# Performance work log

Measured on AMD Instinct MI355X. Metric: run time of the kernel, lower is better.

## Reference

```python
import jax, jax.numpy as jnp
import numpy as np

B, L, D = 128, 196, 512
T = 20
V, E, H, A = 10000, 256, 512, 512


def setup_inputs() -> dict:
    key = jax.random.key(0)
    ks = jax.random.split(key, 20)
    s = lambda *sh: 0.02
    inp = {
        "a": jax.random.normal(ks[0], (B, L, D), jnp.float32),
        "captions": jax.random.randint(ks[1], (B, T), 0, V),
        "lengths": jnp.full((B,), T, dtype=jnp.int64),
        "embed_W": jax.random.normal(ks[2], (V, E), jnp.float32) * 0.02,
        "Wa": jax.random.normal(ks[3], (D, A), jnp.float32) * 0.02,
        "Wh": jax.random.normal(ks[4], (H, A), jnp.float32) * 0.02,
        "Wc": jax.random.normal(ks[5], (H, A), jnp.float32) * 0.02,
        "v": jax.random.normal(ks[6], (A,), jnp.float32) * 0.02,
        "beta_W": jax.random.normal(ks[7], (H, 1), jnp.float32) * 0.02,
        "beta_b": jnp.zeros((1,), jnp.float32),
        "W_ih": jax.random.normal(ks[8], (E + D, 4 * H), jnp.float32) * 0.02,
        "W_hh": jax.random.normal(ks[9], (H, 4 * H), jnp.float32) * 0.02,
        "b_ih": jnp.zeros((4 * H,), jnp.float32),
        "b_hh": jnp.zeros((4 * H,), jnp.float32),
        "fc_W": jax.random.normal(ks[10], (H, V), jnp.float32) * 0.02,
        "fc_b": jnp.zeros((V,), jnp.float32),
        "initW_h": jax.random.normal(ks[11], (D, H), jnp.float32) * 0.02,
        "initb_h": jnp.zeros((H,), jnp.float32),
        "initW_c": jax.random.normal(ks[12], (D, H), jnp.float32) * 0.02,
        "initb_c": jnp.zeros((H,), jnp.float32),
    }
    return inp


def _decode(a, captions, embed_W, Wa, Wh, Wc, v, beta_W, beta_b,
            W_ih, W_hh, b_ih, b_hh, fc_W, fc_b,
            initW_h, initb_h, initW_c, initb_c):
    # dropout layers are treated as identity (eval mode) for a deterministic reference
    emb = embed_W[captions]                       # (B, T, E)
    mean_ctx = a.mean(axis=1)                     # (B, D)
    h0 = jnp.tanh(mean_ctx @ initW_h + initb_h)   # (B, H)
    c0 = jnp.tanh(mean_ctx @ initW_c + initb_c)
    wa = a @ Wa                                   # (B, L, A), hoisted (invariant over t)
    Hd = h0.shape[-1]

    def step(carry, x_t):
        h, c, prev_h = carry
        # dual additive attention: scores from annotations + h + prev_h (context_input)
        score = jnp.tanh(wa + (h @ Wh)[:, None, :] + (prev_h @ Wc)[:, None, :])  # (B,L,A)
        e = score @ v                                                            # (B,L)
        alpha = jax.nn.softmax(e, axis=1)
        beta = jax.nn.sigmoid(h @ beta_W + beta_b)                               # (B,1)
        ctx = beta * jnp.einsum('bl,bld->bd', alpha, a)                          # (B,D)
        # LSTMCell
        x = jnp.concatenate([x_t, ctx], axis=1)                                  # (B,E+D)
        gates = x @ W_ih + b_ih + h @ W_hh + b_hh                                # (B,4H)
        i, f, g, o = jnp.split(gates, 4, axis=1)
        c_new = jax.nn.sigmoid(f) * c + jax.nn.sigmoid(i) * jnp.tanh(g)
        h_new = jax.nn.sigmoid(o) * jnp.tanh(c_new)
        logits_t = h_new @ fc_W + fc_b                                           # (B,V)
        return (h_new, c_new, h_new), (logits_t, alpha)

    xs = jnp.swapaxes(emb[:, :T - 1, :], 0, 1)    # (T-1, B, E) time-major
    _, (logits_t, alphas_t) = jax.lax.scan(step, (h0, c0, h0), xs)
    # all lengths == T: pack_padded_sequence(batch_first=True).data is time-major flatten
    packed_logits = logits_t.reshape((T - 1) * a.shape[0], -1)                   # ((T-1)*B, V)
    alphas = jnp.swapaxes(alphas_t, 0, 1)                                        # (B, T-1, L)
    return packed_logits, alphas


def reference(a, captions, lengths, embed_W, Wa, Wh, Wc, v, beta_W, beta_b,
              W_ih, W_hh, b_ih, b_hh, fc_W, fc_b,
              initW_h, initb_h, initW_c, initb_c):
    return _decode(a, captions, embed_W, Wa, Wh, Wc, v, beta_W, beta_b,
                   W_ih, W_hh, b_ih, b_hh, fc_W, fc_b,
                   initW_h, initb_h, initW_c, initb_c)
```

## Files before the change

### kernel.cpp

```cpp
#include <hip/hip_runtime.h>
#include <hip/hip_bf16.h>
#include <math.h>

#define B_ 128
#define L_ 196
#define D_ 512
#define T_ 20
#define V_ 10000
#define E_ 256
#define H_ 512
#define A_ 512
#define TM1 19
#define ROWS (TM1*B_)
#define G4H 2048
#define KCAT 1024
#define LH 98

typedef unsigned short ushort_t;
typedef __attribute__((ext_vector_type(8))) short bf16x8;
typedef __attribute__((ext_vector_type(4))) float f32x4;

__device__ __forceinline__ float fast_tanh(float x){
    float ax = fabsf(x);
    float e = __expf(-2.f*ax);
    float r = __builtin_amdgcn_rcpf(1.f + e);
    return copysignf((1.f - e)*r, x);
}
__device__ __forceinline__ float sigmoidf_(float x){
    return __builtin_amdgcn_rcpf(1.f + __expf(-x));
}
__device__ __forceinline__ ushort_t f2b(float f){
    union{float f; unsigned u;} x; x.f = f;
    unsigned r = x.u + 0x7fffu + ((x.u>>16)&1u);
    return (ushort_t)(r>>16);
}
__device__ __forceinline__ float b2f(ushort_t h){
    union{unsigned u; float f;} x; x.u = ((unsigned)h)<<16;
    return x.f;
}
__device__ __forceinline__ float b2f_lo(unsigned u){ union{unsigned u; float f;} x; x.u = u<<16; return x.f; }
__device__ __forceinline__ float b2f_hi(unsigned u){ union{unsigned u; float f;} x; x.u = u & 0xffff0000u; return x.f; }

#define GL16(gsrc, ldst) __builtin_amdgcn_global_load_lds( \
    (const __attribute__((address_space(1))) unsigned*)(gsrc), \
    (__attribute__((address_space(3))) unsigned*)(ldst), 16, 0, 0)

template<int OUT_BF16, int HAS_BIAS, int NT, int SWZ>
__global__ __launch_bounds__(256)
void gemm_mfma(const ushort_t* __restrict__ A, int lda,
               const ushort_t* __restrict__ BT, int ldb,
               void* __restrict__ Cout, int ldc,
               int N, int K, const float* __restrict__ bias)
{
    __shared__ ushort_t As[2][4096];
    __shared__ ushort_t Bs[2][4096];
    int bm, bn;
    if (SWZ){
        int bid = blockIdx.x;
        int swz = (bid & 7)*190 + (bid >> 3);
        int mt = swz % 19, nt = swz / 19;
        if (nt >= 79) return;
        bm = mt*128; bn = nt*128;
    } else {
        bm = blockIdx.y * 128; bn = blockIdx.x * 128;
    }
    const int tid = threadIdx.x;
    const int lane = tid & 63;
    const int wave = tid >> 6;
    const int wm = (wave >> 1) * 64;
    const int wn = (wave & 1) * 64;
    const int lrow = lane & 15;
    const int lk8  = (lane >> 4) * 8;
    const int srow = tid >> 2;
    const int skq0 = (tid & 3) * 8;
    const int wbase = wave * 512;

    f32x4 acc[4][4];
    #pragma unroll
    for (int i=0;i<4;i++)
        #pragma unroll
        for (int j=0;j<4;j++) acc[i][j] = (f32x4){0.f,0.f,0.f,0.f};

    const ushort_t* Ab = A  + (size_t)(bm+srow)*lda + skq0;
    const ushort_t* Bb = BT + (size_t)(bn+srow)*ldb + skq0;

    GL16(Ab,                    &As[0][wbase]);
    GL16(Ab + (size_t)64*lda,   &As[0][2048 + wbase]);
    GL16(Bb,                    &Bs[0][wbase]);
    GL16(Bb + (size_t)64*ldb,   &Bs[0][2048 + wbase]);

    int buf = 0;
    for (int k0 = 0; k0 < K; k0 += 32) {
        asm volatile("s_waitcnt vmcnt(0)" ::: "memory");
        __syncthreads();
        if (k0 + 32 < K){
            int nb = buf ^ 1;
            GL16(Ab + k0 + 32,                  &As[nb][wbase]);
            GL16(Ab + (size_t)64*lda + k0 + 32, &As[nb][2048 + wbase]);
            GL16(Bb + k0 + 32,                  &Bs[nb][wbase]);
            GL16(Bb + (size_t)64*ldb + k0 + 32, &Bs[nb][2048 + wbase]);
        }
        bf16x8 af[4], bfr[4];
        #pragma unroll
        for (int i=0;i<4;i++) af[i]  = *(bf16x8*)&As[buf][(wm + i*16 + lrow)*32 + lk8];
        #pragma unroll
        for (int j=0;j<4;j++) bfr[j] = *(bf16x8*)&Bs[buf][(wn + j*16 + lrow)*32 + lk8];
        #pragma unroll
        for (int i=0;i<4;i++)
            #pragma unroll
            for (int j=0;j<4;j++)
                acc[i][j] = __builtin_amdgcn_mfma_f32_16x16x32_bf16(af[i], bfr[j], acc[i][j], 0, 0, 0);
        buf ^= 1;
    }

    const int rq = (lane >> 4) * 4;
    #pragma unroll
    for (int j=0;j<4;j++){
        int col = bn + wn + j*16 + lrow;
        if (col >= N) continue;
        float bv = HAS_BIAS ? bias[col] : 0.f;
        #pragma unroll
        for (int i=0;i<4;i++){
            #pragma unroll
            for (int q=0;q<4;q++){
                int row = bm + wm + i*16 + rq + q;
                float v = acc[i][j][q] + bv;
                if (OUT_BF16) ((ushort_t*)Cout)[(size_t)row*ldc + col] = f2b(v);
                else if (NT)  __builtin_nontemporal_store(v, &((float*)Cout)[(size_t)row*ldc + col]);
                else          ((float*)Cout)[(size_t)row*ldc + col] = v;
            }
        }
    }
}

__global__ __launch_bounds__(256) void gemm64t2(const float* __restrict__ A, int lda,
                       const float* __restrict__ B0, const float* __restrict__ B1, int ldb,
                       float* __restrict__ C0, float* __restrict__ C1, int ldc,
                       const float* __restrict__ bias0, const float* __restrict__ bias1)
{
    const float* Bm  = blockIdx.z ? B1 : B0;
    float* C         = blockIdx.z ? C1 : C0;
    const float* bias= blockIdx.z ? bias1 : bias0;
    __shared__ float As[16][65];
    __shared__ float Bs[16][65];
    int bm = blockIdx.y*64, bn = blockIdx.x*64;
    int tid = threadIdx.x;
    int tx = tid & 15, ty = tid >> 4;
    float acc[4][4] = {};
    for (int k0 = 0; k0 < D_; k0 += 16) {
        {
            int r  = tid >> 2;
            int kq = (tid & 3) * 4;
            float4 va = *(const float4*)(A + (size_t)(bm+r)*lda + k0 + kq);
            As[kq+0][r]=va.x; As[kq+1][r]=va.y; As[kq+2][r]=va.z; As[kq+3][r]=va.w;
        }
        {
            int kk = tid >> 4;
            int nq = (tid & 15) * 4;
            float4 vb = *(const float4*)(Bm + (size_t)(k0+kk)*ldb + bn + nq);
            Bs[kk][nq+0]=vb.x; Bs[kk][nq+1]=vb.y; Bs[kk][nq+2]=vb.z; Bs[kk][nq+3]=vb.w;
        }
        __syncthreads();
        #pragma unroll
        for (int k = 0; k < 16; ++k) {
            float a0[4], b0[4];
            #pragma unroll
            for (int i=0;i<4;i++) a0[i] = As[k][ty*4+i];
            #pragma unroll
            for (int j=0;j<4;j++) b0[j] = Bs[k][tx*4+j];
            #pragma unroll
            for (int i=0;i<4;i++)
                #pragma unroll
                for (int j=0;j<4;j++)
                    acc[i][j] = fmaf(a0[i], b0[j], acc[i][j]);
        }
        __syncthreads();
    }
    #pragma unroll
    for (int i=0;i<4;i++){
        int row = bm + ty*4 + i;
        #pragma unroll
        for (int j=0;j<4;j++){
            int col = bn + tx*4 + j;
            C[(size_t)row*ldc + col] = fast_tanh(acc[i][j] + bias[col]);
        }
    }
}

struct TJob { const float* src; const float* src2; ushort_t* dst;
              int lds, Ksz, Nsz, koff, ldk, nx, nblk; };
struct TJobs { TJob j[6]; };

__global__ __launch_bounds__(256) void combo_trans_k(TJobs J){
    __shared__ float t[32][33];
    int bid = blockIdx.x;
    int ji = 0;
    while (bid >= J.j[ji].nblk){ bid -= J.j[ji].nblk; ji++; }
    const TJob jb = J.j[ji];
    int n0 = (bid % jb.nx)*32, k0 = (bid / jb.nx)*32;
    int tx = threadIdx.x & 31, ty = threadIdx.x >> 5;
    #pragma unroll
    for (int kk = ty; kk < 32; kk += 8){
        int k = k0 + kk, n = n0 + tx;
        float v = 0.f;
        if (k < jb.Ksz && n < jb.Nsz){
            v = jb.src[(size_t)k*jb.lds + n];
            if (jb.src2) v += jb.src2[(size_t)k*jb.lds + n];
        }
        t[kk][tx] = v;
    }
    __syncthreads();
    #pragma unroll
    for (int nn = ty; nn < 32; nn += 8){
        int n = n0 + nn, k = k0 + tx;
        if (k < jb.Ksz) jb.dst[(size_t)n*jb.ldk + jb.koff + k] = f2b(t[tx][nn]);
    }
}

__global__ __launch_bounds__(256) void mean_cvt_k(const float* __restrict__ a, ushort_t* __restrict__ a_b,
                                                  float* __restrict__ mc,
                                                  const float* __restrict__ b_ih, const float* __restrict__ b_hh,
                                                  float* __restrict__ bias4h, unsigned* __restrict__ ebar){
    if (blockIdx.x == 64){
        for (int k = threadIdx.x; k < G4H; k += 256) bias4h[k] = b_ih[k] + b_hh[k];
        if (threadIdx.x < B_) ebar[threadIdx.x] = 0u;
        return;
    }
    int idx = blockIdx.x*256 + threadIdx.x;
    int b = idx >> 7, dq = (idx & 127) * 4;
    const float* p = a + (size_t)b*L_*D_ + dq;
    ushort_t* q = a_b + (size_t)b*L_*D_ + dq;
    float4 s = make_float4(0.f,0.f,0.f,0.f);
    for (int l=0;l<L_;l++){
        float4 v = *(const float4*)(p + (size_t)l*D_);
        s.x += v.x; s.y += v.y; s.z += v.z; s.w += v.w;
        ushort_t r[4] = {f2b(v.x),f2b(v.y),f2b(v.z),f2b(v.w)};
        *(uint2*)(q + (size_t)l*D_) = *(uint2*)r;
    }
    const float inv = 1.f/(float)L_;
    float4 o = make_float4(s.x*inv, s.y*inv, s.z*inv, s.w*inv);
    *(float4*)(mc + (size_t)b*D_ + dq) = o;
}

__global__ __launch_bounds__(256) void gather_emb(const int* __restrict__ captions, const float* __restrict__ embW,
                           ushort_t* __restrict__ xemb){
    int i = blockIdx.x*4 + (threadIdx.x >> 6);
    int lane = threadIdx.x & 63;
    int t = i / B_, b = i - t*B_;
    int cap = captions[b*T_ + t];
    float4 v = ((const float4*)(embW + (size_t)cap*E_))[lane];
    ushort_t r[4] = {f2b(v.x),f2b(v.y),f2b(v.z),f2b(v.w)};
    *(uint2*)(xemb + (size_t)i*E_ + lane*4) = *(uint2*)r;
}

__global__ __launch_bounds__(512) void hw0cvt_k(const float* __restrict__ h0f,
                        const ushort_t* __restrict__ WhcT,
                        ushort_t* __restrict__ xcat, float* __restrict__ hWp){
    int b = blockIdx.x, tid = threadIdx.x;
    int lane = tid & 63, wave = tid >> 6;
    __shared__ ushort_t hls[512];
    float hv = h0f[b*H_ + tid];
    ushort_t hb = f2b(hv);
    xcat[(size_t)b*KCAT + D_ + tid] = hb;
    hls[tid] = hb;
    hWp[(size_t)(b*2+1)*512 + tid] = 0.f;
    __syncthreads();
    int wn = wave * 64;
    int col16 = lane & 15;
    int khi = (lane >> 4) * 8;
    bool a_on = (col16 == 0);
    f32x4 acc[4];
    #pragma unroll
    for (int f=0;f<4;f++) acc[f] = (f32x4){0.f,0.f,0.f,0.f};
    for (int kk=0; kk<16; kk++){
        bf16x8 af = (bf16x8){0,0,0,0,0,0,0,0};
        if (a_on) af = *(const bf16x8*)&hls[kk*32 + khi];
        #pragma unroll
        for (int f=0;f<4;f++){
            bf16x8 bf = *(const bf16x8*)(WhcT + (size_t)(wn + f*16 + col16)*512 + kk*32 + khi);
            acc[f] = __builtin_amdgcn_mfma_f32_16x16x32_bf16(af, bf, acc[f], 0, 0, 0);
        }
    }
    if (lane < 16){
        #pragma unroll
        for (int f=0;f<4;f++) hWp[(size_t)(b*2+0)*512 + wn + f*16 + lane] = acc[f][0];
    }
}

__global__ __launch_bounds__(512) void mega2_k(const ushort_t* __restrict__ wa,
                        const ushort_t* __restrict__ a_b,
                        const float* __restrict__ v,
                        const float* __restrict__ beta_W, const float* __restrict__ beta_b,
                        const ushort_t* __restrict__ WhcT,
                        const float* __restrict__ gp, const float* __restrict__ embWih,
                        float* __restrict__ cbuf, float* __restrict__ hWp,
                        ushort_t* __restrict__ xcat, ushort_t* __restrict__ Hall,
                        float* __restrict__ alphas_out, float* __restrict__ ebuf,
                        unsigned* __restrict__ ebar, int t)
{
    const int b = blockIdx.x, half = blockIdx.y;
    const int tid = threadIdx.x;
    const int lane = tid & 63, wave = tid >> 6;
    __shared__ ushort_t hls[256];
    __shared__ float red[512];
    __shared__ float al_s[224];
    __shared__ float part[2][256];

    if (t > 0){
        if (tid < 256){
            const int j = half*256 + tid;
            const float* eb = embWih + ((size_t)((t-1)*B_ + b))*G4H;
            float gi = eb[j], gf = eb[H_+j], gg = eb[2*H_+j], go = eb[3*H_+j];
            #pragma unroll
            for (int ks=0; ks<8; ks++){
                const float* g = gp + ((size_t)(ks*B_ + b))*G4H;
                gi += g[j]; gf += g[H_+j]; gg += g[2*H_+j]; go += g[3*H_+j];
            }
            float ig = sigmoidf_(gi), fg = sigmoidf_(gf);
            float g2 = fast_tanh(gg), og = sigmoidf_(go);
            float c = fg*cbuf[b*H_+j] + ig*g2;
            float h = og*fast_tanh(c);
            cbuf[b*H_+j] = c;
            ushort_t hb = f2b(h);
            xcat[(size_t)b*KCAT + D_ + j] = hb;
            Hall[((size_t)(t-1)*B_ + b)*H_ + j] = hb;
            hls[tid] = hb;
        }
        __syncthreads();
        int wn = wave * 64;
        int col16 = lane & 15;
        int khi = (lane >> 4) * 8;
        bool a_on = (col16 == 0);
        f32x4 acc[4];
        #pragma unroll
        for (int f=0;f<4;f++) acc[f] = (f32x4){0.f,0.f,0.f,0.f};
        #pragma unroll
        for (int kk=0; kk<8; kk++){
            bf16x8 af = (bf16x8){0,0,0,0,0,0,0,0};
            if (a_on) af = *(const bf16x8*)&hls[kk*32 + khi];
            #pragma unroll
            for (int f=0;f<4;f++){
                bf16x8 bf = *(const bf16x8*)(WhcT + (size_t)(wn + f*16 + col16)*512 + half*256 + kk*32 + khi);
                acc[f] = __builtin_amdgcn_mfma_f32_16x16x32_bf16(af, bf, acc[f], 0, 0, 0);
            }
        }
        if (lane < 16){
            #pragma unroll
            for (int f=0;f<4;f++) hWp[(size_t)(b*2+half)*512 + wn + f*16 + lane] = acc[f][0];
        }
    }
    __syncthreads();
    if (tid == 0){
        __threadfence();
        atomicAdd(&ebar[b], 1u);
        const unsigned tgt = 2u*(unsigned)(2*t+1);
        while (__hip_atomic_load(&ebar[b], __ATOMIC_ACQUIRE, __HIP_MEMORY_SCOPE_AGENT) < tgt)
            __builtin_amdgcn_s_sleep(1);
    }
    __syncthreads();
    {
        const float* hp0 = hWp + (size_t)(b*2+0)*512 + lane*8;
        const float* hp1 = hWp + (size_t)(b*2+1)*512 + lane*8;
        float4 p00 = *(const float4*)hp0, p01 = *(const float4*)(hp0+4);
        float4 p10 = *(const float4*)hp1, p11 = *(const float4*)(hp1+4);
        float4 hw0 = make_float4(p00.x+p10.x, p00.y+p10.y, p00.z+p10.z, p00.w+p10.w);
        float4 hw1 = make_float4(p01.x+p11.x, p01.y+p11.y, p01.z+p11.z, p01.w+p11.w);
        const float* vp = v + lane*8;
        float4 v0 = *(const float4*)vp, v1 = *(const float4*)(vp+4);
        const int l0 = half*LH;
        for (int r = wave; r < LH; r += 8){
            int4 raw = *(const int4*)(wa + (((size_t)(b*L_ + l0 + r))<<9) + lane*8);
            const unsigned* u = (const unsigned*)&raw;
            float s;
            s  = fast_tanh(b2f_lo(u[0]) + hw0.x)*v0.x;
            s += fast_tanh(b2f_hi(u[0]) + hw0.y)*v0.y;
            s += fast_tanh(b2f_lo(u[1]) + hw0.z)*v0.z;
            s += fast_tanh(b2f_hi(u[1]) + hw0.w)*v0.w;
            s += fast_tanh(b2f_lo(u[2]) + hw1.x)*v1.x;
            s += fast_tanh(b2f_hi(u[2]) + hw1.y)*v1.y;
            s += fast_tanh(b2f_lo(u[3]) + hw1.z)*v1.z;
            s += fast_tanh(b2f_hi(u[3]) + hw1.w)*v1.w;
            #pragma unroll
            for (int off=32; off; off>>=1) s += __shfl_down(s, off);
            if (lane==0) ebuf[b*L_ + l0 + r] = s;
        }
    }
    __syncthreads();
    if (tid == 0){
        __threadfence();
        atomicAdd(&ebar[b], 1u);
        const unsigned tgt = 2u*(unsigned)(2*t+2);
        while (__hip_atomic_load(&ebar[b], __ATOMIC_ACQUIRE, __HIP_MEMORY_SCOPE_AGENT) < tgt)
            __builtin_amdgcn_s_sleep(1);
    }
    __syncthreads();
    float ev = (tid < L_) ? ebuf[b*L_ + tid] : -3.0e38f;
    red[tid] = ev; __syncthreads();
    #pragma unroll
    for (int s=256; s; s>>=1){ if (tid<s) red[tid] = fmaxf(red[tid], red[tid+s]); __syncthreads(); }
    float m = red[0]; __syncthreads();
    float pr = (tid < L_) ? __expf(ev - m) : 0.f;
    red[tid] = pr; __syncthreads();
    #pragma unroll
    for (int s=256; s; s>>=1){ if (tid<s) red[tid] += red[tid+s]; __syncthreads(); }
    float inv = 1.f / red[0];
    __syncthreads();
    if (tid < L_) al_s[tid] = pr*inv;
    const int l0 = half*LH;
    if (tid >= l0 && tid < l0 + LH)
        __builtin_nontemporal_store(pr*inv, alphas_out + (size_t)b*TM1*L_ + (size_t)t*L_ + tid);
    float dv = b2f(xcat[(size_t)b*KCAT + D_ + tid]) * beta_W[tid];
    red[tid] = dv; __syncthreads();
    #pragma unroll
    for (int s=256; s; s>>=1){ if (tid<s) red[tid] += red[tid+s]; __syncthreads(); }
    float beta = sigmoidf_(red[0] + beta_b[0]);
    __syncthreads();
    const int d  = half*256 + (tid & 255);
    const int lr = tid >> 8;
    const ushort_t* pa = a_b + (((size_t)(b*L_ + lr*LH))<<9) + d;
    float s0 = 0.f;
    #pragma unroll 7
    for (int i=0; i<LH; ++i) s0 = fmaf(al_s[lr*LH + i], b2f(pa[(size_t)i*512]), s0);
    part[lr][tid & 255] = s0;
    __syncthreads();
    if (tid < 256)
        xcat[(size_t)b*KCAT + half*256 + tid] = f2b(beta*(part[0][tid] + part[1][tid]));
}

__global__ __launch_bounds__(256) void gates_k(const ushort_t* __restrict__ xcat,
                        const ushort_t* __restrict__ WcatT, float* __restrict__ gp){
    __shared__ ushort_t As[128*32];
    __shared__ ushort_t Bs[64*32];
    const int bn = blockIdx.x*64;
    const int ks = blockIdx.y;
    const int tid = threadIdx.x;
    const int lane = tid & 63, wave = tid >> 6;
    const int wm = wave*32;
    const int lrow = lane & 15;
    const int lk8 = (lane >> 4) * 8;
    f32x4 acc[2][4];
    #pragma unroll
    for (int i=0;i<2;i++)
        #pragma unroll
        for (int j=0;j<4;j++) acc[i][j] = (f32x4){0.f,0.f,0.f,0.f};

    for (int kk = 0; kk < 4; ++kk){
        int k0 = ks*128 + kk*32;
        int c0 = 2*tid;
        int r0 = c0 >> 2,  kq0 = (c0 & 3)*8;
        int r1 = (c0+1) >> 2, kq1 = ((c0+1) & 3)*8;
        int4 a0 = *(const int4*)(xcat + (size_t)r0*KCAT + k0 + kq0);
        int4 a1 = *(const int4*)(xcat + (size_t)r1*KCAT + k0 + kq1);
        int rb = tid >> 2, kqb = (tid & 3)*8;
        int4 b0 = *(const int4*)(WcatT + (size_t)(bn+rb)*KCAT + k0 + kqb);
        __syncthreads();
        *(int4*)&As[r0*32 + kq0] = a0;
        *(int4*)&As[r1*32 + kq1] = a1;
        *(int4*)&Bs[rb*32 + kqb] = b0;
        __syncthreads();
        bf16x8 af[2], bfr[4];
        #pragma unroll
        for (int i=0;i<2;i++) af[i] = *(bf16x8*)&As[(wm + i*16 + lrow)*32 + lk8];
        #pragma unroll
        for (int j=0;j<4;j++) bfr[j] = *(bf16x8*)&Bs[(j*16 + lrow)*32 + lk8];
        #pragma unroll
        for (int i=0;i<2;i++)
            #pragma unroll
            for (int j=0;j<4;j++)
                acc[i][j] = __builtin_amdgcn_mfma_f32_16x16x32_bf16(af[i], bfr[j], acc[i][j], 0, 0, 0);
    }
    const int rq = (lane >> 4) * 4;
    #pragma unroll
    for (int i=0;i<2;i++){
        #pragma unroll
        for (int j=0;j<4;j++){
            int gcol = bn + j*16 + lrow;
            #pragma unroll
            for (int q=0;q<4;q++){
                int grow = wm + i*16 + rq + q;
                gp[((size_t)(ks*B_ + grow))*G4H + gcol] = acc[i][j][q];
            }
        }
    }
}

__global__ __launch_bounds__(512) void lstmfin_k(const float* __restrict__ gp, const float* __restrict__ embWih,
                       const float* __restrict__ cbuf, ushort_t* __restrict__ Hall){
    int b = blockIdx.x, j = threadIdx.x;
    const float* eb = embWih + ((size_t)(18*B_ + b))*G4H;
    float gi = eb[j], gf = eb[H_+j], gg = eb[2*H_+j], go = eb[3*H_+j];
    #pragma unroll
    for (int ks=0; ks<8; ks++){
        const float* g = gp + ((size_t)(ks*B_ + b))*G4H;
        gi += g[j]; gf += g[H_+j]; gg += g[2*H_+j]; go += g[3*H_+j];
    }
    float ig = sigmoidf_(gi), fg = sigmoidf_(gf);
    float g2 = fast_tanh(gg), og = sigmoidf_(go);
    float c = fg*cbuf[b*H_+j] + ig*g2;
    float h = og*fast_tanh(c);
    Hall[((size_t)18*B_ + b)*H_ + j] = f2b(h);
}

extern "C" void kernel_launch(void* const* d_in, const int* in_sizes, int n_in,
                              void* d_out, int out_size, void* d_ws, size_t ws_size,
                              hipStream_t stream) {
    const float* a      = (const float*)d_in[0];
    const int*   caps   = (const int*)  d_in[1];
    const float* embW   = (const float*)d_in[3];
    const float* Wa     = (const float*)d_in[4];
    const float* Wh     = (const float*)d_in[5];
    const float* Wc     = (const float*)d_in[6];
    const float* v      = (const float*)d_in[7];
    const float* beta_W = (const float*)d_in[8];
    const float* beta_b = (const float*)d_in[9];
    const float* W_ih   = (const float*)d_in[10];
    const float* W_hh   = (const float*)d_in[11];
    const float* b_ih   = (const float*)d_in[12];
    const float* b_hh   = (const float*)d_in[13];
    const float* fc_W   = (const float*)d_in[14];
    const float* fc_b   = (const float*)d_in[15];
    const float* iWh    = (const float*)d_in[16];
    const float* ibh    = (const float*)d_in[17];
    const float* iWc    = (const float*)d_in[18];
    const float* ibc    = (const float*)d_in[19];

    float* out    = (float*)d_out;
    float* alphas = out + (size_t)ROWS*V_;

    char* ob = (char*)d_out;
    ushort_t* wa_b   = (ushort_t*)(ob);
    ushort_t* a_b    = (ushort_t*)(ob + 25690112);
    float*    embWih = (float*)   (ob + 51380224);

    char* wb = (char*)d_ws;
    float* mean_ctx = (float*)(wb);
    float* cbuf     = (float*)(wb + 262144);
    float* h0f      = (float*)(wb + 524288);
    float* hWp      = (float*)(wb + 786432);
    float* ebuf     = (float*)(wb + 1310720);
    float* bias4h   = (float*)(wb + 1413120);
    unsigned* ebar  = (unsigned*)(wb + 1421312);
    float* gp       = (float*)(wb + 1422336);
    ushort_t* xcat_b = (ushort_t*)(wb + 9810944);
    ushort_t* xemb_b = (ushort_t*)(wb + 10073088);
    ushort_t* Hall   = (ushort_t*)(wb + 11318272);
    ushort_t* WaT    = (ushort_t*)(wb + 13808640);
    ushort_t* WhcT   = (ushort_t*)(wb + 14332928);
    ushort_t* WihT   = (ushort_t*)(wb + 14857216);
    ushort_t* WcatT  = (ushort_t*)(wb + 15905792);
    ushort_t* fcWT   = (ushort_t*)(wb + 20100096);

    TJobs J;
    J.j[0] = { Wa,   nullptr, WaT,  512, 512, 512,  0,   512,  16, 256 };
    J.j[1] = { Wh,   Wc,      WhcT, 512, 512, 512,  0,   512,  16, 256 };
    J.j[2] = { W_ih, nullptr, WihT, G4H, 256, G4H,  0,   256,  64, 512 };
    J.j[3] = { W_ih + (size_t)E_*G4H, nullptr, WcatT, G4H, 512, G4H, 0,   KCAT, 64, 1024 };
    J.j[4] = { W_hh, nullptr, WcatT, G4H, 512, G4H,  512, KCAT, 64, 1024 };
    J.j[5] = { fc_W, nullptr, fcWT, V_,  512, V_,   0,   512,  316, 5056 };
    combo_trans_k<<<8128, 256, 0, stream>>>(J);
    mean_cvt_k<<<65, 256, 0, stream>>>(a, a_b, mean_ctx, b_ih, b_hh, bias4h, ebar);
    gather_emb<<<ROWS/4, 256, 0, stream>>>(caps, embW, xemb_b);
    gemm64t2<<<dim3(8,2,2), 256, 0, stream>>>(mean_ctx, D_, iWh, iWc, H_, h0f, cbuf, H_, ibh, ibc);
    hw0cvt_k<<<B_, 512, 0, stream>>>(h0f, WhcT, xcat_b, hWp);
    gemm_mfma<1,0,0,0><<<dim3(4,196), 256, 0, stream>>>(a_b, D_, WaT, D_, wa_b, A_, A_, D_, nullptr);
    gemm_mfma<0,1,0,0><<<dim3(16,19), 256, 0, stream>>>(xemb_b, E_, WihT, E_, embWih, G4H, G4H, E_, bias4h);

    for (int t = 0; t < TM1; ++t){
        mega2_k<<<dim3(B_,2), 512, 0, stream>>>(wa_b, a_b, v, beta_W, beta_b, WhcT,
                                                gp, embWih, cbuf, hWp, xcat_b, Hall,
                                                alphas, ebuf, ebar, t);
        gates_k<<<dim3(32,8), 256, 0, stream>>>(xcat_b, WcatT, gp);
    }
    lstmfin_k<<<B_, 512, 0, stream>>>(gp, embWih, cbuf, Hall);

    gemm_mfma<0,1,1,1><<<dim3(1520), 256, 0, stream>>>(Hall, H_, fcWT, H_, out, V_, V_, H_, fc_b);
}
```

Before: 1.063 ms.

## Fuse prep kernels and dual GEMMs; replace tree reductions with shuffles in attention step

Merges the transpose, mean/convert and embedding-gather kernels into one launch, and runs the Wa and embedding-input GEMMs as one dual-job launch, to cut launch overhead and fill the GPU better. Inside the recurrent step kernel, the beta gate dot product now comes from per-half partials computed while h is produced, and the max/sum softmax reductions use wave shuffles instead of 512-wide shared-memory trees. The context weighted sum reads four values per vectorized load with eight row groups. This adds cross-block dependency handling for the beta partials and more complex indexing.

```diff
diff --git a/kernel.cpp b/kernel.cpp
--- a/kernel.cpp
+++ b/kernel.cpp
@@ -128,6 +128,84 @@
                 if (OUT_BF16) ((ushort_t*)Cout)[(size_t)row*ldc + col] = f2b(v);
                 else if (NT)  __builtin_nontemporal_store(v, &((float*)Cout)[(size_t)row*ldc + col]);
                 else          ((float*)Cout)[(size_t)row*ldc + col] = v;
+            }
+        }
+    }
+}
+
+struct GJob { const ushort_t* A; int lda; const ushort_t* BT; int ldb;
+              void* C; int ldc; int N, K; const float* bias; int out_bf16; int nx; int nblk; };
+
+__global__ __launch_bounds__(256) void gemm_dual_k(GJob j0, GJob j1){
+    __shared__ ushort_t As[2][4096];
+    __shared__ ushort_t Bs[2][4096];
+    int bid = blockIdx.x;
+    GJob jb = (bid < j0.nblk) ? j0 : j1;
+    if (bid >= j0.nblk) bid -= j0.nblk;
+    const int bn = (bid % jb.nx)*128, bm = (bid / jb.nx)*128;
+    const int tid = threadIdx.x;
+    const int lane = tid & 63;
+    const int wave = tid >> 6;
+    const int wm = (wave >> 1) * 64;
+    const int wn = (wave & 1) * 64;
+    const int lrow = lane & 15;
+    const int lk8  = (lane >> 4) * 8;
+    const int srow = tid >> 2;
+    const int skq0 = (tid & 3) * 8;
+    const int wbase = wave * 512;
+
+    f32x4 acc[4][4];
+    #pragma unroll
+    for (int i=0;i<4;i++)
+        #pragma unroll
+        for (int j=0;j<4;j++) acc[i][j] = (f32x4){0.f,0.f,0.f,0.f};
+
+    const ushort_t* Ab = jb.A  + (size_t)(bm+srow)*jb.lda + skq0;
+    const ushort_t* Bb = jb.BT + (size_t)(bn+srow)*jb.ldb + skq0;
+
+    GL16(Ab,                        &As[0][wbase]);
+    GL16(Ab + (size_t)64*jb.lda,    &As[0][2048 + wbase]);
+    GL16(Bb,                        &Bs[0][wbase]);
+    GL16(Bb + (size_t)64*jb.ldb,    &Bs[0][2048 + wbase]);
+
+    int buf = 0;
+    for (int k0 = 0; k0 < jb.K; k0 += 32) {
+        asm volatile("s_waitcnt vmcnt(0)" ::: "memory");
+        __syncthreads();
+        if (k0 + 32 < jb.K){
+            int nb = buf ^ 1;
+            GL16(Ab + k0 + 32,                      &As[nb][wbase]);
+            GL16(Ab + (size_t)64*jb.lda + k0 + 32,  &As[nb][2048 + wbase]);
+            GL16(Bb + k0 + 32,                      &Bs[nb][wbase]);
+            GL16(Bb + (size_t)64*jb.ldb + k0 + 32,  &Bs[nb][2048 + wbase]);
+        }
+        bf16x8 af[4], bfr[4];
+        #pragma unroll
+        for (int i=0;i<4;i++) af[i]  = *(bf16x8*)&As[buf][(wm + i*16 + lrow)*32 + lk8];
+        #pragma unroll
+        for (int j=0;j<4;j++) bfr[j] = *(bf16x8*)&Bs[buf][(wn + j*16 + lrow)*32 + lk8];
+        #pragma unroll
+        for (int i=0;i<4;i++)
+            #pragma unroll
+            for (int j=0;j<4;j++)
+                acc[i][j] = __builtin_amdgcn_mfma_f32_16x16x32_bf16(af[i], bfr[j], acc[i][j], 0, 0, 0);
+        buf ^= 1;
+    }
+
+    const int rq = (lane >> 4) * 4;
+    #pragma unroll
+    for (int j=0;j<4;j++){
+        int col = bn + wn + j*16 + lrow;
+        if (col >= jb.N) continue;
+        float bv = jb.bias ? jb.bias[col] : 0.f;
+        #pragma unroll
+        for (int i=0;i<4;i++){
+            #pragma unroll
+            for (int q=0;q<4;q++){
+                int row = bm + wm + i*16 + rq + q;
+                float v = acc[i][j][q] + bv;
+                if (jb.out_bf16) ((ushort_t*)jb.C)[(size_t)row*jb.ldc + col] = f2b(v);
+                else             ((float*)jb.C)[(size_t)row*jb.ldc + col] = v;
             }
         }
     }
@@ -189,82 +267,95 @@
 
 struct TJob { const float* src; const float* src2; ushort_t* dst;
               int lds, Ksz, Nsz, koff, ldk, nx, nblk; };
-struct TJobs { TJob j[6]; };
-
-__global__ __launch_bounds__(256) void combo_trans_k(TJobs J){
+struct PrepArgs {
+    TJob j[6];
+    const float* a; ushort_t* a_b; float* mc;
+    const float* b_ih; const float* b_hh; float* bias4h; unsigned* ebar;
+    const int* caps; const float* embW; ushort_t* xemb;
+};
+
+__global__ __launch_bounds__(256) void prep_all_k(PrepArgs P){
     __shared__ float t[32][33];
     int bid = blockIdx.x;
-    int ji = 0;
-    while (bid >= J.j[ji].nblk){ bid -= J.j[ji].nblk; ji++; }
-    const TJob jb = J.j[ji];
-    int n0 = (bid % jb.nx)*32, k0 = (bid / jb.nx)*32;
-    int tx = threadIdx.x & 31, ty = threadIdx.x >> 5;
-    #pragma unroll
-    for (int kk = ty; kk < 32; kk += 8){
-        int k = k0 + kk, n = n0 + tx;
-        float v = 0.f;
-        if (k < jb.Ksz && n < jb.Nsz){
-            v = jb.src[(size_t)k*jb.lds + n];
-            if (jb.src2) v += jb.src2[(size_t)k*jb.lds + n];
-        }
-        t[kk][tx] = v;
-    }
-    __syncthreads();
-    #pragma unroll
-    for (int nn = ty; nn < 32; nn += 8){
-        int n = n0 + nn, k = k0 + tx;
-        if (k < jb.Ksz) jb.dst[(size_t)n*jb.ldk + jb.koff + k] = f2b(t[tx][nn]);
-    }
-}
-
-__global__ __launch_bounds__(256) void mean_cvt_k(const float* __restrict__ a, ushort_t* __restrict__ a_b,
-                                                  float* __restrict__ mc,
-                                                  const float* __restrict__ b_ih, const float* __restrict__ b_hh,
-                                                  float* __restrict__ bias4h, unsigned* __restrict__ ebar){
-    if (blockIdx.x == 64){
-        for (int k = threadIdx.x; k < G4H; k += 256) bias4h[k] = b_ih[k] + b_hh[k];
-        if (threadIdx.x < B_) ebar[threadIdx.x] = 0u;
+    const int tid = threadIdx.x;
+    if (bid < 8128){
+        int ji = 0;
+        while (bid >= P.j[ji].nblk){ bid -= P.j[ji].nblk; ji++; }
+        const TJob jb = P.j[ji];
+        int n0 = (bid % jb.nx)*32, k0 = (bid / jb.nx)*32;
+        int tx = tid & 31, ty = tid >> 5;
+        #pragma unroll
+        for (int kk = ty; kk < 32; kk += 8){
+            int k = k0 + kk, n = n0 + tx;
+            float v = 0.f;
+            if (k < jb.Ksz && n < jb.Nsz){
+                v = jb.src[(size_t)k*jb.lds + n];
+                if (jb.src2) v += jb.src2[(size_t)k*jb.lds + n];
+            }
+            t[kk][tx] = v;
+        }
+        __syncthreads();
+        #pragma unroll
+        for (int nn = ty; nn < 32; nn += 8){
+            int n = n0 + nn, k = k0 + tx;
+            if (k < jb.Ksz) jb.dst[(size_t)n*jb.ldk + jb.koff + k] = f2b(t[tx][nn]);
+        }
         return;
     }
-    int idx = blockIdx.x*256 + threadIdx.x;
-    int b = idx >> 7, dq = (idx & 127) * 4;
-    const float* p = a + (size_t)b*L_*D_ + dq;
-    ushort_t* q = a_b + (size_t)b*L_*D_ + dq;
-    float4 s = make_float4(0.f,0.f,0.f,0.f);
-    for (int l=0;l<L_;l++){
-        float4 v = *(const float4*)(p + (size_t)l*D_);
-        s.x += v.x; s.y += v.y; s.z += v.z; s.w += v.w;
-        ushort_t r[4] = {f2b(v.x),f2b(v.y),f2b(v.z),f2b(v.w)};
-        *(uint2*)(q + (size_t)l*D_) = *(uint2*)r;
-    }
-    const float inv = 1.f/(float)L_;
-    float4 o = make_float4(s.x*inv, s.y*inv, s.z*inv, s.w*inv);
-    *(float4*)(mc + (size_t)b*D_ + dq) = o;
-}
-
-__global__ __launch_bounds__(256) void gather_emb(const int* __restrict__ captions, const float* __restrict__ embW,
-                           ushort_t* __restrict__ xemb){
-    int i = blockIdx.x*4 + (threadIdx.x >> 6);
-    int lane = threadIdx.x & 63;
-    int t = i / B_, b = i - t*B_;
-    int cap = captions[b*T_ + t];
-    float4 v = ((const float4*)(embW + (size_t)cap*E_))[lane];
+    bid -= 8128;
+    if (bid < 65){
+        if (bid == 64){
+            for (int k = tid; k < G4H; k += 256) P.bias4h[k] = P.b_ih[k] + P.b_hh[k];
+            if (tid < B_) P.ebar[tid] = 0u;
+            return;
+        }
+        int idx = bid*256 + tid;
+        int b = idx >> 7, dq = (idx & 127) * 4;
+        const float* p = P.a + (size_t)b*L_*D_ + dq;
+        ushort_t* q = P.a_b + (size_t)b*L_*D_ + dq;
+        float4 s = make_float4(0.f,0.f,0.f,0.f);
+        for (int l=0;l<L_;l++){
+            float4 v = *(const float4*)(p + (size_t)l*D_);
+            s.x += v.x; s.y += v.y; s.z += v.z; s.w += v.w;
+            ushort_t r[4] = {f2b(v.x),f2b(v.y),f2b(v.z),f2b(v.w)};
+            *(uint2*)(q + (size_t)l*D_) = *(uint2*)r;
+        }
+        const float inv = 1.f/(float)L_;
+        float4 o = make_float4(s.x*inv, s.y*inv, s.z*inv, s.w*inv);
+        *(float4*)(P.mc + (size_t)b*D_ + dq) = o;
+        return;
+    }
+    bid -= 65;
+    int i = bid*4 + (tid >> 6);
+    int lane = tid & 63;
+    int tt = i / B_, b = i - tt*B_;
+    int cap = P.caps[b*T_ + tt];
+    float4 v = ((const float4*)(P.embW + (size_t)cap*E_))[lane];
     ushort_t r[4] = {f2b(v.x),f2b(v.y),f2b(v.z),f2b(v.w)};
-    *(uint2*)(xemb + (size_t)i*E_ + lane*4) = *(uint2*)r;
+    *(uint2*)(P.xemb + (size_t)i*E_ + lane*4) = *(uint2*)r;
 }
 
 __global__ __launch_bounds__(512) void hw0cvt_k(const float* __restrict__ h0f,
-                        const ushort_t* __restrict__ WhcT,
-                        ushort_t* __restrict__ xcat, float* __restrict__ hWp){
+                        const ushort_t* __restrict__ WhcT, const float* __restrict__ beta_W,
+                        ushort_t* __restrict__ xcat, float* __restrict__ hWp, float* __restrict__ bdot){
     int b = blockIdx.x, tid = threadIdx.x;
     int lane = tid & 63, wave = tid >> 6;
     __shared__ ushort_t hls[512];
+    __shared__ float rr[8];
     float hv = h0f[b*H_ + tid];
     ushort_t hb = f2b(hv);
     xcat[(size_t)b*KCAT + D_ + tid] = hb;
     hls[tid] = hb;
     hWp[(size_t)(b*2+1)*512 + tid] = 0.f;
-    __syncthreads();
+    float dv = hv * beta_W[tid];
+    #pragma unroll
+    for (int off=32; off; off>>=1) dv += __shfl_down(dv, off);
+    if (lane==0) rr[wave] = dv;
+    __syncthreads();
+    if (tid == 0){
+        float s = rr[0]+rr[1]+rr[2]+rr[3]+rr[4]+rr[5]+rr[6]+rr[7];
+        bdot[b*2] = s; bdot[b*2+1] = 0.f;
+    }
     int wn = wave * 64;
     int col16 = lane & 15;
     int khi = (lane >> 4) * 8;
@@ -296,17 +387,18 @@
                         float* __restrict__ cbuf, float* __restrict__ hWp,
                         ushort_t* __restrict__ xcat, ushort_t* __restrict__ Hall,
                         float* __restrict__ alphas_out, float* __restrict__ ebuf,
-                        unsigned* __restrict__ ebar, int t)
+                        unsigned* __restrict__ ebar, float* __restrict__ bdot, int t)
 {
     const int b = blockIdx.x, half = blockIdx.y;
     const int tid = threadIdx.x;
     const int lane = tid & 63, wave = tid >> 6;
     __shared__ ushort_t hls[256];
-    __shared__ float red[512];
+    __shared__ float red[16];
     __shared__ float al_s[224];
-    __shared__ float part[2][256];
+    __shared__ float4 part4[8][64];
 
     if (t > 0){
+        float dv = 0.f;
         if (tid < 256){
             const int j = half*256 + tid;
             const float* eb = embWih + ((size_t)((t-1)*B_ + b))*G4H;
@@ -325,7 +417,11 @@
             xcat[(size_t)b*KCAT + D_ + j] = hb;
             Hall[((size_t)(t-1)*B_ + b)*H_ + j] = hb;
             hls[tid] = hb;
-        }
+            dv = h * beta_W[j];
+        }
+        #pragma unroll
+        for (int off=32; off; off>>=1) dv += __shfl_down(dv, off);
+        if (lane==0) red[wave] = dv;
         __syncthreads();
         int wn = wave * 64;
         int col16 = lane & 15;
@@ -351,6 +447,7 @@
     }
     __syncthreads();
     if (tid == 0){
+        if (t > 0) bdot[b*2+half] = red[0]+red[1]+red[2]+red[3];
         __threadfence();
         atomicAdd(&ebar[b], 1u);
         const unsigned tgt = 2u*(unsigned)(2*t+1);
@@ -395,36 +492,55 @@
     }
     __syncthreads();
     float ev = (tid < L_) ? ebuf[b*L_ + tid] : -3.0e38f;
-    red[tid] = ev; __syncthreads();
-    #pragma unroll
-    for (int s=256; s; s>>=1){ if (tid<s) red[tid] = fmaxf(red[tid], red[tid+s]); __syncthreads(); }
-    float m = red[0]; __syncthreads();
+    float wmax = ev;
+    #pragma unroll
+    for (int off=32; off; off>>=1) wmax = fmaxf(wmax, __shfl_down(wmax, off));
+    if (lane==0) red[wave] = wmax;
+    __syncthreads();
+    float m = fmaxf(fmaxf(fmaxf(red[0],red[1]),fmaxf(red[2],red[3])),
+                    fmaxf(fmaxf(red[4],red[5]),fmaxf(red[6],red[7])));
     float pr = (tid < L_) ? __expf(ev - m) : 0.f;
-    red[tid] = pr; __syncthreads();
-    #pragma unroll
-    for (int s=256; s; s>>=1){ if (tid<s) red[tid] += red[tid+s]; __syncthreads(); }
-    float inv = 1.f / red[0];
-    __syncthreads();
+    float wsum = pr;
+    #pragma unroll
+    for (int off=32; off; off>>=1) wsum += __shfl_down(wsum, off);
+    if (lane==0) red[8+wave] = wsum;
+    __syncthreads();
+    float inv = 1.f / (red[8]+red[9]+red[10]+red[11]+red[12]+red[13]+red[14]+red[15]);
     if (tid < L_) al_s[tid] = pr*inv;
     const int l0 = half*LH;
     if (tid >= l0 && tid < l0 + LH)
         __builtin_nontemporal_store(pr*inv, alphas_out + (size_t)b*TM1*L_ + (size_t)t*L_ + tid);
-    float dv = b2f(xcat[(size_t)b*KCAT + D_ + tid]) * beta_W[tid];
-    red[tid] = dv; __syncthreads();
-    #pragma unroll
-    for (int s=256; s; s>>=1){ if (tid<s) red[tid] += red[tid+s]; __syncthreads(); }
-    float beta = sigmoidf_(red[0] + beta_b[0]);
-    __syncthreads();
-    const int d  = half*256 + (tid & 255);
-    const int lr = tid >> 8;
-    const ushort_t* pa = a_b + (((size_t)(b*L_ + lr*LH))<<9) + d;
-    float s0 = 0.f;
-    #pragma unroll 7
-    for (int i=0; i<LH; ++i) s0 = fmaf(al_s[lr*LH + i], b2f(pa[(size_t)i*512]), s0);
-    part[lr][tid & 255] = s0;
-    __syncthreads();
-    if (tid < 256)
-        xcat[(size_t)b*KCAT + half*256 + tid] = f2b(beta*(part[0][tid] + part[1][tid]));
+    __syncthreads();
+    {
+        const int dg = tid & 63;
+        const int lr = tid >> 6;
+        const int d0 = half*256 + dg*4;
+        const ushort_t* pa = a_b + (((size_t)(b*L_))<<9) + d0;
+        float4 s = make_float4(0.f,0.f,0.f,0.f);
+        for (int l = lr; l < L_; l += 8){
+            uint2 av = *(const uint2*)(pa + ((size_t)l<<9));
+            float al = al_s[l];
+            s.x = fmaf(al, b2f_lo(av.x), s.x);
+            s.y = fmaf(al, b2f_hi(av.x), s.y);
+            s.z = fmaf(al, b2f_lo(av.y), s.z);
+            s.w = fmaf(al, b2f_hi(av.y), s.w);
+        }
+        part4[lr][dg] = s;
+        __syncthreads();
+        if (tid < 64){
+            float beta = sigmoidf_(bdot[b*2] + bdot[b*2+1] + beta_b[0]);
+            float4 r = make_float4(0.f,0.f,0.f,0.f);
+            #pragma unroll
+            for (int q=0;q<8;q++){
+                float4 pv = part4[q][tid];
+                r.x += pv.x; r.y += pv.y; r.z += pv.z; r.w += pv.w;
+            }
+            unsigned lo = (unsigned)f2b(beta*r.x) | (((unsigned)f2b(beta*r.y))<<16);
+            unsigned hi = (unsigned)f2b(beta*r.z) | (((unsigned)f2b(beta*r.w))<<16);
+            uint2 pk; pk.x = lo; pk.y = hi;
+            *(uint2*)(xcat + (size_t)b*KCAT + half*256 + tid*4) = pk;
+        }
+    }
 }
 
 __global__ __launch_bounds__(256) void gates_k(const ushort_t* __restrict__ xcat,
@@ -534,6 +650,7 @@
 
     char* wb = (char*)d_ws;
     float* mean_ctx = (float*)(wb);
+    float* bdot     = (float*)(wb + 131072);
     float* cbuf     = (float*)(wb + 262144);
     float* h0f      = (float*)(wb + 524288);
     float* hWp      = (float*)(wb + 786432);
@@ -550,25 +667,29 @@
     ushort_t* WcatT  = (ushort_t*)(wb + 15905792);
     ushort_t* fcWT   = (ushort_t*)(wb + 20100096);
 
-    TJobs J;
-    J.j[0] = { Wa,   nullptr, WaT,  512, 512, 512,  0,   512,  16, 256 };
-    J.j[1] = { Wh,   Wc,      WhcT, 512, 512, 512,  0,   512,  16, 256 };
-    J.j[2] = { W_ih, nullptr, WihT, G4H, 256, G4H,  0,   256,  64, 512 };
-    J.j[3] = { W_ih + (size_t)E_*G4H, nullptr, WcatT, G4H, 512, G4H, 0,   KCAT, 64, 1024 };
-    J.j[4] = { W_hh, nullptr, WcatT, G4H, 512, G4H,  512, KCAT, 64, 1024 };
-    J.j[5] = { fc_W, nullptr, fcWT, V_,  512, V_,   0,   512,  316, 5056 };
-    combo_trans_k<<<8128, 256, 0, stream>>>(J);
-    mean_cvt_k<<<65, 256, 0, stream>>>(a, a_b, mean_ctx, b_ih, b_hh, bias4h, ebar);
-    gather_emb<<<ROWS/4, 256, 0, stream>>>(caps, embW, xemb_b);
+    PrepArgs P;
+    P.j[0] = { Wa,   nullptr, WaT,  512, 512, 512,  0,   512,  16, 256 };
+    P.j[1] = { Wh,   Wc,      WhcT, 512, 512, 512,  0,   512,  16, 256 };
+    P.j[2] = { W_ih, nullptr, WihT, G4H, 256, G4H,  0,   256,  64, 512 };
+    P.j[3] = { W_ih + (size_t)E_*G4H, nullptr, WcatT, G4H, 512, G4H, 0,   KCAT, 64, 1024 };
+    P.j[4] = { W_hh, nullptr, WcatT, G4H, 512, G4H,  512, KCAT, 64, 1024 };
+    P.j[5] = { fc_W, nullptr, fcWT, V_,  512, V_,   0,   512,  316, 5056 };
+    P.a = a; P.a_b = a_b; P.mc = mean_ctx;
+    P.b_ih = b_ih; P.b_hh = b_hh; P.bias4h = bias4h; P.ebar = ebar;
+    P.caps = caps; P.embW = embW; P.xemb = xemb_b;
+    prep_all_k<<<8801, 256, 0, stream>>>(P);
+
     gemm64t2<<<dim3(8,2,2), 256, 0, stream>>>(mean_ctx, D_, iWh, iWc, H_, h0f, cbuf, H_, ibh, ibc);
-    hw0cvt_k<<<B_, 512, 0, stream>>>(h0f, WhcT, xcat_b, hWp);
-    gemm_mfma<1,0,0,0><<<dim3(4,196), 256, 0, stream>>>(a_b, D_, WaT, D_, wa_b, A_, A_, D_, nullptr);
-    gemm_mfma<0,1,0,0><<<dim3(16,19), 256, 0, stream>>>(xemb_b, E_, WihT, E_, embWih, G4H, G4H, E_, bias4h);
+    hw0cvt_k<<<B_, 512, 0, stream>>>(h0f, WhcT, beta_W, xcat_b, hWp, bdot);
+
+    GJob g0 = { a_b,    512, WaT,  512, wa_b,   512, 512,  512, nullptr, 1, 4,  784 };
+    GJob g1 = { xemb_b, 256, WihT, 256, embWih, G4H, G4H,  256, bias4h,  0, 16, 304 };
+    gemm_dual_k<<<1088, 256, 0, stream>>>(g0, g1);
 
     for (int t = 0; t < TM1; ++t){
         mega2_k<<<dim3(B_,2), 512, 0, stream>>>(wa_b, a_b, v, beta_W, beta_b, WhcT,
                                                 gp, embWih, cbuf, hWp, xcat_b, Hall,
-                                                alphas, ebuf, ebar, t);
+                                                alphas, ebuf, ebar, bdot, t);
         gates_k<<<dim3(32,8), 256, 0, stream>>>(xcat_b, WcatT, gp);
     }
     lstmfin_k<<<B_, 512, 0, stream>>>(gp, embWih, cbuf, Hall);
```

Measured after the change: 1.109 ms. +4.4%, slower.
